# Performance work log

Measured on AMD Instinct MI355X. Metric: run time of the kernel, lower is better.

Reference implementation:

```python
import jax, jax.numpy as jnp
import numpy as np

B, N1, N2, D = 8, 2048, 2048, 512

def setup_inputs() -> dict:
    key = jax.random.key(0)
    k1, k2, k3, k4 = jax.random.split(key, 4)
    input1 = jax.random.normal(k1, (B, N1, D), dtype=jnp.float32)
    input2 = jax.random.normal(k2, (B, N2, D), dtype=jnp.float32)
    # nn.Linear(D, D): weight [D, D] (out, in), bias [D]
    W_w = jax.random.normal(k3, (D, D), dtype=jnp.float32) * (1.0 / np.sqrt(D))
    W_b = jax.random.normal(k4, (D,), dtype=jnp.float32) * 0.01
    return {"input1": input1, "input2": input2, "W_w": W_w, "W_b": W_b}

def reference(input1, input2, W_w, W_b):
    # q = W(input1): [B, N1, D]
    q = jnp.einsum('bnd,od->bno', input1, W_w) + W_b
    # unscaled scores softmax over last dim (keys N2)
    attn = jax.nn.softmax(jnp.einsum('bnd,bmd->bnm', q, input2), axis=-1)  # [B, N1, N2]
    output1 = jnp.einsum('bnm,bmd->bnd', attn, input2)   # [B, N1, D]
    output2 = jnp.einsum('bnm,bnd->bmd', attn, input1)   # attn^T @ input1 -> [B, N2, D]
    return (output1, output2)
```

## Files before the change

kernel.cpp:

```cpp
#include <hip/hip_runtime.h>


typedef _Float16 f16x8 __attribute__((ext_vector_type(8)));
typedef _Float16 f16x4 __attribute__((ext_vector_type(4)));
typedef float floatx4 __attribute__((ext_vector_type(4)));
typedef __attribute__((address_space(1))) const void* gptr_t;
typedef __attribute__((address_space(3))) void* lptr_t;

union F8 { f16x8 v; _Float16 h[8]; unsigned short u[8]; unsigned w[4]; };
union F4 { f16x4 v; _Float16 h[4]; unsigned u2[2]; };

__device__ __forceinline__ void gld16(const void* g, void* l) {
    __builtin_amdgcn_global_load_lds((gptr_t)g, (lptr_t)l, 16, 0, 0);
}
__device__ __forceinline__ floatx4 mfma16(f16x8 a, f16x8 b, floatx4 c) {
    return __builtin_amdgcn_mfma_f32_16x16x32_f16(a, b, c, 0, 0, 0);
}

template <int ROWS>
__device__ __forceinline__ void stage64(const _Float16* g, int ldg,
                                        _Float16* lds, int tid) {
#pragma unroll
    for (int c = 0; c < (ROWS * 8) / 256; ++c) {
        const int q = c * 256 + tid;
        const int row = q >> 3;
        const int oct = (q & 7) ^ (row & 7);
        gld16(g + (size_t)row * ldg + oct * 8, lds + q * 8);
    }
}
__device__ __forceinline__ f16x8 ldfrag64(const _Float16* lds, int row, int j) {
    return *(const f16x8*)&lds[row * 64 + ((j ^ (row & 7)) << 3)];
}
__device__ __forceinline__ f16x8 ldfragA(const _Float16* lds, int row, int j) {
    return *(const f16x8*)&lds[row * 64 + ((j ^ ((row >> 1) & 7)) << 3)];
}

#define TS 66
__global__ __launch_bounds__(256) void k_prep2(
    const float* __restrict__ in1, const float* __restrict__ in2,
    _Float16* __restrict__ x16, _Float16* __restrict__ xt,
    _Float16* __restrict__ k16, _Float16* __restrict__ vt)
{
    __shared__ __align__(16) _Float16 T[64 * TS];
    const int z = blockIdx.z;
    const int b = z & 7;
    const float* src = (z < 8 ? in1 : in2);
    _Float16* rowo = (z < 8 ? x16 : k16);
    _Float16* colo = (z < 8 ? xt : vt);
    const int d0 = blockIdx.x * 64, n0 = blockIdx.y * 64;
    const float* Sp = src + (size_t)b * 2048 * 512;
    _Float16* Rp = rowo + (size_t)b * 2048 * 512;
    _Float16* Cp = colo + (size_t)b * 512 * 2048;
    const int t = threadIdx.x;

#pragma unroll
    for (int c = 0; c < 4; c++) {
        const int q = c * 256 + t, r = q >> 4, c4 = q & 15;
        const float4 g = *(const float4*)(Sp + (size_t)(n0 + r) * 512 + d0 + c4 * 4);
        F4 w;
        w.h[0] = (_Float16)g.x; w.h[1] = (_Float16)g.y;
        w.h[2] = (_Float16)g.z; w.h[3] = (_Float16)g.w;
        *(f16x4*)(Rp + (size_t)(n0 + r) * 512 + d0 + c4 * 4) = w.v;
        *(unsigned*)&T[r * TS + c4 * 4]     = w.u2[0];
        *(unsigned*)&T[r * TS + c4 * 4 + 2] = w.u2[1];
    }
    __syncthreads();
    const int c8 = t & 7, drp = (t >> 3) * 2;
    F8 w0, w1;
#pragma unroll
    for (int i = 0; i < 8; i++) {
        const unsigned g = *(const unsigned*)&T[(c8 * 8 + i) * TS + drp];
        w0.u[i] = (unsigned short)(g & 0xffffu);
        w1.u[i] = (unsigned short)(g >> 16);
    }
    *(f16x8*)(Cp + (size_t)(d0 + drp) * 2048 + n0 + c8 * 8) = w0.v;
    *(f16x8*)(Cp + (size_t)(d0 + drp + 1) * 2048 + n0 + c8 * 8) = w1.v;
}

__global__ __launch_bounds__(256) void k_cvt(const float* __restrict__ src,
                                             _Float16* __restrict__ dst)
{
    const size_t i = ((size_t)blockIdx.x * 256 + threadIdx.x) * 8;
    float4 a = *(const float4*)(src + i);
    float4 b = *(const float4*)(src + i + 4);
    F8 w;
    w.h[0] = (_Float16)a.x; w.h[1] = (_Float16)a.y;
    w.h[2] = (_Float16)a.z; w.h[3] = (_Float16)a.w;
    w.h[4] = (_Float16)b.x; w.h[5] = (_Float16)b.y;
    w.h[6] = (_Float16)b.z; w.h[7] = (_Float16)b.w;
    *(f16x8*)(dst + i) = w.v;
}

__global__ __launch_bounds__(256, 4) void k_qgemm16(
    const _Float16* __restrict__ A, const _Float16* __restrict__ W,
    const float* __restrict__ bias, _Float16* __restrict__ q)
{
    __shared__ __align__(16) _Float16 As[128 * 64], Bs[128 * 64];
    const int tid = threadIdx.x;
    const int lane = tid & 63, wave = tid >> 6;
    const int wM = (wave >> 1) * 64, wN = (wave & 1) * 64;
    const int lrow = lane & 15, kq = lane >> 4;
    const int bi = blockIdx.x;
    const int r0 = (bi >> 2) * 128, c0 = (bi & 3) * 128;

    floatx4 acc[4][4];
#pragma unroll
    for (int i = 0; i < 4; i++)
#pragma unroll
        for (int j = 0; j < 4; j++) acc[i][j] = (floatx4){0.f, 0.f, 0.f, 0.f};

    for (int k0 = 0; k0 < 512; k0 += 64) {
        stage64<128>(A + (size_t)r0 * 512 + k0, 512, As, tid);
        stage64<128>(W + (size_t)c0 * 512 + k0, 512, Bs, tid);
        __syncthreads();
#pragma unroll
        for (int ks = 0; ks < 2; ks++) {
            f16x8 a[4], b[4];
#pragma unroll
            for (int i = 0; i < 4; i++) {
                a[i] = ldfrag64(As, wM + i * 16 + lrow, ks * 4 + kq);
                b[i] = ldfrag64(Bs, wN + i * 16 + lrow, ks * 4 + kq);
            }
#pragma unroll
            for (int mi = 0; mi < 4; mi++)
#pragma unroll
                for (int ni = 0; ni < 4; ni++)
                    acc[mi][ni] = mfma16(a[mi], b[ni], acc[mi][ni]);
        }
        __syncthreads();
    }
#pragma unroll
    for (int ni = 0; ni < 4; ni++) {
        const int col = c0 + wN + ni * 16 + lrow;
        const float bv = bias[col];
#pragma unroll
        for (int mi = 0; mi < 4; mi++) {
            const int row = r0 + wM + mi * 16 + kq * 4;
#pragma unroll
            for (int r = 0; r < 4; r++)
                q[(size_t)(row + r) * 512 + col] = (_Float16)(acc[mi][ni][r] + bv);
        }
    }
}

__global__ __launch_bounds__(256, 4) void k_scores16(
    const _Float16* __restrict__ q, const _Float16* __restrict__ k,
    _Float16* __restrict__ S)
{
    __shared__ __align__(16) _Float16 As[128 * 64], Bs[128 * 64];
    const int tid = threadIdx.x;
    const int lane = tid & 63, wave = tid >> 6;
    const int wM = (wave >> 1) * 64, wN = (wave & 1) * 64;
    const int lrow = lane & 15, kq = lane >> 4;
    const int bi = blockIdx.x;
    const int bz = bi & 7, t = bi >> 3;
    const int c0 = (t & 15) * 128, r0 = (t >> 4) * 128;
    const _Float16* qp = q + (size_t)bz * 2048 * 512;
    const _Float16* kp = k + (size_t)bz * 2048 * 512;
    _Float16* Sp = S + (size_t)bz * 2048 * 2048;

    floatx4 acc[4][4];
#pragma unroll
    for (int i = 0; i < 4; i++)
#pragma unroll
        for (int j = 0; j < 4; j++) acc[i][j] = (floatx4){0.f, 0.f, 0.f, 0.f};

    for (int k0 = 0; k0 < 512; k0 += 64) {
        stage64<128>(qp + (size_t)r0 * 512 + k0, 512, As, tid);
        stage64<128>(kp + (size_t)c0 * 512 + k0, 512, Bs, tid);
        __syncthreads();
#pragma unroll
        for (int ks = 0; ks < 2; ks++) {
            f16x8 a[4], b[4];
#pragma unroll
            for (int i = 0; i < 4; i++) {
                a[i] = ldfrag64(As, wM + i * 16 + lrow, ks * 4 + kq);
                b[i] = ldfrag64(Bs, wN + i * 16 + lrow, ks * 4 + kq);
            }
#pragma unroll
            for (int mi = 0; mi < 4; mi++)
#pragma unroll
                for (int ni = 0; ni < 4; ni++)
                    acc[mi][ni] = mfma16(a[mi], b[ni], acc[mi][ni]);
        }
        __syncthreads();
    }
#pragma unroll
    for (int mi = 0; mi < 4; mi++)
#pragma unroll
        for (int ni = 0; ni < 4; ni++) {
            const int row = r0 + wM + mi * 16 + kq * 4;
            const int col = c0 + wN + ni * 16 + lrow;
            _Float16* dst = Sp + (size_t)row * 2048 + col;
#pragma unroll
            for (int r = 0; r < 4; r++) dst[(size_t)r * 2048] = (_Float16)acc[mi][ni][r];
        }
}

__global__ __launch_bounds__(256) void k_softmax(const _Float16* __restrict__ S,
                                                 _Float16* __restrict__ P)
{
    const int wave = threadIdx.x >> 6, lane = threadIdx.x & 63;
    const int row = blockIdx.x * 4 + wave;
    const _Float16* s = S + (size_t)row * 2048;
    _Float16* p = P + (size_t)row * 2048;

    F8 raw[4];
    float v[32];
#pragma unroll
    for (int c = 0; c < 4; c++) {
        raw[c].v = *(const f16x8*)(s + c * 512 + lane * 8);
#pragma unroll
        for (int i = 0; i < 8; i++) v[c * 8 + i] = (float)raw[c].h[i];
    }
    float m = v[0];
#pragma unroll
    for (int i = 1; i < 32; i++) m = fmaxf(m, v[i]);
#pragma unroll
    for (int off = 32; off >= 1; off >>= 1) m = fmaxf(m, __shfl_xor(m, off));

    float sum = 0.f;
#pragma unroll
    for (int i = 0; i < 32; i++) { v[i] = __expf(v[i] - m); sum += v[i]; }
#pragma unroll
    for (int off = 32; off >= 1; off >>= 1) sum += __shfl_xor(sum, off);
    const float inv = 1.0f / sum;

#pragma unroll
    for (int c = 0; c < 4; c++) {
        F8 w;
#pragma unroll
        for (int i = 0; i < 8; i++) w.h[i] = (_Float16)(v[c * 8 + i] * inv);
        *(f16x8*)(p + c * 512 + lane * 8) = w.v;
    }
}

__device__ __forceinline__ void loadtr16(const _Float16* Pp, int r0, int mPair,
                                         int kBase, int k0, unsigned (&u)[16]) {
#pragma unroll
    for (int j = 0; j < 16; j++)
        u[j] = *(const unsigned*)(
            Pp + (size_t)(k0 + kBase + j) * 2048 + r0 + mPair);
}

__global__ __launch_bounds__(256, 2) void k_out12(
    const _Float16* __restrict__ P, const _Float16* __restrict__ Vt,
    const _Float16* __restrict__ Xt, float* __restrict__ O1,
    float* __restrict__ O2)
{
    __shared__ __align__(16) _Float16 lds[24576];
    const int tid = threadIdx.x;
    const int lane = tid & 63, wave = tid >> 6;
    const int wM = (wave >> 1) * 64, wN = (wave & 1) * 128;
    const int lrow = lane & 15, kq = lane >> 4;
    const bool isO2 = blockIdx.x & 1;
    const int bi = blockIdx.x >> 1;
    const int bz = bi & 7, t = bi >> 3;
    const int c0 = (t & 1) * 256, r0 = (t >> 1) * 128;
    const _Float16* Pp = P + (size_t)bz * 2048 * 2048;
    const _Float16* Bp = (isO2 ? Xt : Vt) + (size_t)bz * 512 * 2048;
    float* Op = (isO2 ? O2 : O1) + (size_t)bz * 2048 * 512;

    floatx4 acc[4][8];
#pragma unroll
    for (int i = 0; i < 4; i++)
#pragma unroll
        for (int j = 0; j < 8; j++) acc[i][j] = (floatx4){0.f, 0.f, 0.f, 0.f};

    if (!isO2) {
        for (int k0 = 0; k0 < 2048; k0 += 64) {
            stage64<128>(Pp + (size_t)r0 * 2048 + k0, 2048, lds, tid);
            stage64<256>(Bp + (size_t)c0 * 2048 + k0, 2048, lds + 8192, tid);
            __syncthreads();
#pragma unroll
            for (int ks = 0; ks < 2; ks++) {
                f16x8 a[4], b[8];
#pragma unroll
                for (int i = 0; i < 4; i++)
                    a[i] = ldfrag64(lds, wM + i * 16 + lrow, ks * 4 + kq);
#pragma unroll
                for (int i = 0; i < 8; i++)
                    b[i] = ldfrag64(lds + 8192, wN + i * 16 + lrow, ks * 4 + kq);
#pragma unroll
                for (int mi = 0; mi < 4; mi++)
#pragma unroll
                    for (int ni = 0; ni < 8; ni++)
                        acc[mi][ni] = mfma16(a[mi], b[ni], acc[mi][ni]);
            }
            __syncthreads();
        }
    } else {
        _Float16* As_ = lds;
        const int mPair = (tid & 63) * 2;
        const int kBase = (tid >> 6) * 16;

        unsigned u[16];
        loadtr16(Pp, r0, mPair, kBase, 0, u);
        for (int k0 = 0; k0 < 2048; k0 += 64) {
            const int sw = (mPair >> 1) & 7;
#pragma unroll
            for (int half = 0; half < 2; half++) {
                const int oct = (kBase >> 3) + half;
                F8 w0, w1;
#pragma unroll
                for (int j = 0; j < 8; j++) {
                    const unsigned g = u[half * 8 + j];
                    w0.u[j] = (unsigned short)(g & 0xffffu);
                    w1.u[j] = (unsigned short)(g >> 16);
                }
                *(f16x8*)&As_[mPair * 64 + ((oct ^ sw) << 3)] = w0.v;
                *(f16x8*)&As_[(mPair + 1) * 64 + ((oct ^ sw) << 3)] = w1.v;
            }
            stage64<256>(Bp + (size_t)c0 * 2048 + k0, 2048, lds + 8192, tid);
            __syncthreads();
            if (k0 < 2048 - 64)
                loadtr16(Pp, r0, mPair, kBase, k0 + 64, u);
#pragma unroll
            for (int ks = 0; ks < 2; ks++) {
                f16x8 a[4], b[8];
#pragma unroll
                for (int i = 0; i < 4; i++)
                    a[i] = ldfragA(As_, wM + i * 16 + lrow, ks * 4 + kq);
#pragma unroll
                for (int i = 0; i < 8; i++)
                    b[i] = ldfrag64(lds + 8192, wN + i * 16 + lrow, ks * 4 + kq);
#pragma unroll
                for (int mi = 0; mi < 4; mi++)
#pragma unroll
                    for (int ni = 0; ni < 8; ni++)
                        acc[mi][ni] = mfma16(a[mi], b[ni], acc[mi][ni]);
            }
            __syncthreads();
        }
    }
#pragma unroll
    for (int mi = 0; mi < 4; mi++)
#pragma unroll
        for (int ni = 0; ni < 8; ni++) {
            const int row = r0 + wM + mi * 16 + kq * 4;
            const int col = c0 + wN + ni * 16 + lrow;
            float* dst = Op + (size_t)row * 512 + col;
#pragma unroll
            for (int r = 0; r < 4; r++) dst[(size_t)r * 512] = acc[mi][ni][r];
        }
}

extern "C" void kernel_launch(void* const* d_in, const int* in_sizes, int n_in,
                              void* d_out, int out_size, void* d_ws, size_t ws_size,
                              hipStream_t stream)
{
    (void)in_sizes; (void)n_in; (void)out_size; (void)ws_size;
    const float* in1 = (const float*)d_in[0];
    const float* in2 = (const float*)d_in[1];
    const float* Ww  = (const float*)d_in[2];
    const float* Wb  = (const float*)d_in[3];
    float* out = (float*)d_out;

    char* ws = (char*)d_ws;
    _Float16* S   = (_Float16*)ws;
    _Float16* P   = (_Float16*)(ws + 67108864ull);
    _Float16* q16 = (_Float16*)(ws + 134217728ull);
    _Float16* x16 = (_Float16*)(ws + 150994944ull);
    _Float16* k16 = (_Float16*)(ws + 167772160ull);
    _Float16* vt  = (_Float16*)(ws + 184549376ull);
    _Float16* xt  = (_Float16*)(ws + 201326592ull);
    _Float16* w16 = (_Float16*)(ws + 218103808ull);

    k_prep2<<<dim3(8, 32, 16), 256, 0, stream>>>(in1, in2, x16, xt, k16, vt);
    k_cvt <<<128, 256, 0, stream>>>(Ww, w16);
    k_qgemm16<<<512, 256, 0, stream>>>(x16, w16, Wb, q16);
    k_scores16<<<2048, 256, 0, stream>>>(q16, k16, S);
    k_softmax<<<4096, 256, 0, stream>>>(S, P);
    k_out12<<<512, 256, 0, stream>>>(P, vt, xt, out, out + 8388608);
}
```

Baseline: 268.1 us.

## Fuse softmax normalization into output GEMMs using per-row max/inverse-sum stats

The softmax kernel now writes only a per-row (max, 1/sum) pair instead of the full normalized P matrix. Both output GEMMs read raw scores S and apply exp and scale while loading fragments. This removes a 64MB write and its re-read of the probability matrix. In exchange, the exponentials are recomputed in both GEMMs, and for each output tile, adding ALU work and per-element stat loads in the transposed O2 path.

```diff
diff --git a/kernel.cpp b/kernel.cpp
--- a/kernel.cpp
+++ b/kernel.cpp
@@ -9,6 +9,7 @@
 
 union F8 { f16x8 v; _Float16 h[8]; unsigned short u[8]; unsigned w[4]; };
 union F4 { f16x4 v; _Float16 h[4]; unsigned u2[2]; };
+union HS { unsigned short s; _Float16 h; };
 
 __device__ __forceinline__ void gld16(const void* g, void* l) {
     __builtin_amdgcn_global_load_lds((gptr_t)g, (lptr_t)l, 16, 0, 0);
@@ -197,13 +198,12 @@
         }
 }
 
-__global__ __launch_bounds__(256) void k_softmax(const _Float16* __restrict__ S,
-                                                 _Float16* __restrict__ P)
+__global__ __launch_bounds__(256) void k_stats(const _Float16* __restrict__ S,
+                                               float2* __restrict__ st)
 {
     const int wave = threadIdx.x >> 6, lane = threadIdx.x & 63;
     const int row = blockIdx.x * 4 + wave;
     const _Float16* s = S + (size_t)row * 2048;
-    _Float16* p = P + (size_t)row * 2048;
 
     F8 raw[4];
     float v[32];
@@ -226,13 +226,7 @@
     for (int off = 32; off >= 1; off >>= 1) sum += __shfl_xor(sum, off);
     const float inv = 1.0f / sum;
 
-#pragma unroll
-    for (int c = 0; c < 4; c++) {
-        F8 w;
-#pragma unroll
-        for (int i = 0; i < 8; i++) w.h[i] = (_Float16)(v[c * 8 + i] * inv);
-        *(f16x8*)(p + c * 512 + lane * 8) = w.v;
-    }
+    if (lane == 0) st[row] = make_float2(m, inv);
 }
 
 __device__ __forceinline__ void loadtr16(const _Float16* Pp, int r0, int mPair,
@@ -244,9 +238,9 @@
 }
 
 __global__ __launch_bounds__(256, 2) void k_out12(
-    const _Float16* __restrict__ P, const _Float16* __restrict__ Vt,
-    const _Float16* __restrict__ Xt, float* __restrict__ O1,
-    float* __restrict__ O2)
+    const _Float16* __restrict__ S, const float2* __restrict__ st,
+    const _Float16* __restrict__ Vt, const _Float16* __restrict__ Xt,
+    float* __restrict__ O1, float* __restrict__ O2)
 {
     __shared__ __align__(16) _Float16 lds[24576];
     const int tid = threadIdx.x;
@@ -257,7 +251,8 @@
     const int bi = blockIdx.x >> 1;
     const int bz = bi & 7, t = bi >> 3;
     const int c0 = (t & 1) * 256, r0 = (t >> 1) * 128;
-    const _Float16* Pp = P + (size_t)bz * 2048 * 2048;
+    const _Float16* Sp = S + (size_t)bz * 2048 * 2048;
+    const float2* sp = st + (size_t)bz * 2048;
     const _Float16* Bp = (isO2 ? Xt : Vt) + (size_t)bz * 512 * 2048;
     float* Op = (isO2 ? O2 : O1) + (size_t)bz * 2048 * 512;
 
@@ -268,16 +263,28 @@
         for (int j = 0; j < 8; j++) acc[i][j] = (floatx4){0.f, 0.f, 0.f, 0.f};
 
     if (!isO2) {
+        float am[4], ai[4];
+#pragma unroll
+        for (int i = 0; i < 4; i++) {
+            const float2 s2 = sp[r0 + wM + i * 16 + lrow];
+            am[i] = s2.x; ai[i] = s2.y;
+        }
         for (int k0 = 0; k0 < 2048; k0 += 64) {
-            stage64<128>(Pp + (size_t)r0 * 2048 + k0, 2048, lds, tid);
+            stage64<128>(Sp + (size_t)r0 * 2048 + k0, 2048, lds, tid);
             stage64<256>(Bp + (size_t)c0 * 2048 + k0, 2048, lds + 8192, tid);
             __syncthreads();
 #pragma unroll
             for (int ks = 0; ks < 2; ks++) {
                 f16x8 a[4], b[8];
 #pragma unroll
-                for (int i = 0; i < 4; i++)
-                    a[i] = ldfrag64(lds, wM + i * 16 + lrow, ks * 4 + kq);
+                for (int i = 0; i < 4; i++) {
+                    F8 ra, pa;
+                    ra.v = ldfrag64(lds, wM + i * 16 + lrow, ks * 4 + kq);
+#pragma unroll
+                    for (int j = 0; j < 8; j++)
+                        pa.h[j] = (_Float16)(__expf((float)ra.h[j] - am[i]) * ai[i]);
+                    a[i] = pa.v;
+                }
 #pragma unroll
                 for (int i = 0; i < 8; i++)
                     b[i] = ldfrag64(lds + 8192, wN + i * 16 + lrow, ks * 4 + kq);
@@ -295,7 +302,7 @@
         const int kBase = (tid >> 6) * 16;
 
         unsigned u[16];
-        loadtr16(Pp, r0, mPair, kBase, 0, u);
+        loadtr16(Sp, r0, mPair, kBase, 0, u);
         for (int k0 = 0; k0 < 2048; k0 += 64) {
             const int sw = (mPair >> 1) & 7;
 #pragma unroll
@@ -305,8 +312,12 @@
 #pragma unroll
                 for (int j = 0; j < 8; j++) {
                     const unsigned g = u[half * 8 + j];
-                    w0.u[j] = (unsigned short)(g & 0xffffu);
-                    w1.u[j] = (unsigned short)(g >> 16);
+                    const float2 s2 = sp[k0 + kBase + half * 8 + j];
+                    HS lo, hi;
+                    lo.s = (unsigned short)(g & 0xffffu);
+                    hi.s = (unsigned short)(g >> 16);
+                    w0.h[j] = (_Float16)(__expf((float)lo.h - s2.x) * s2.y);
+                    w1.h[j] = (_Float16)(__expf((float)hi.h - s2.x) * s2.y);
                 }
                 *(f16x8*)&As_[mPair * 64 + ((oct ^ sw) << 3)] = w0.v;
                 *(f16x8*)&As_[(mPair + 1) * 64 + ((oct ^ sw) << 3)] = w1.v;
@@ -314,7 +325,7 @@
             stage64<256>(Bp + (size_t)c0 * 2048 + k0, 2048, lds + 8192, tid);
             __syncthreads();
             if (k0 < 2048 - 64)
-                loadtr16(Pp, r0, mPair, kBase, k0 + 64, u);
+                loadtr16(Sp, r0, mPair, kBase, k0 + 64, u);
 #pragma unroll
             for (int ks = 0; ks < 2; ks++) {
                 f16x8 a[4], b[8];
@@ -358,7 +369,7 @@
 
     char* ws = (char*)d_ws;
     _Float16* S   = (_Float16*)ws;
-    _Float16* P   = (_Float16*)(ws + 67108864ull);
+    float2*   st  = (float2*)(ws + 67108864ull);
     _Float16* q16 = (_Float16*)(ws + 134217728ull);
     _Float16* x16 = (_Float16*)(ws + 150994944ull);
     _Float16* k16 = (_Float16*)(ws + 167772160ull);
@@ -370,6 +381,6 @@
     k_cvt <<<128, 256, 0, stream>>>(Ww, w16);
     k_qgemm16<<<512, 256, 0, stream>>>(x16, w16, Wb, q16);
     k_scores16<<<2048, 256, 0, stream>>>(q16, k16, S);
-    k_softmax<<<4096, 256, 0, stream>>>(S, P);
-    k_out12<<<512, 256, 0, stream>>>(P, vt, xt, out, out + 8388608);
-}
+    k_stats<<<4096, 256, 0, stream>>>(S, st);
+    k_out12<<<512, 256, 0, stream>>>(S, st, vt, xt, out, out + 8388608);
+}
```

Measured after the change: 307.4 us. +14.7%, slower.
